# Kernel optimization log

Hardware: AMD Instinct MI355X
Metric: run time of the kernel (lower is better)

The kernel has to match this reference:

```python
import math
import jax, jax.numpy as jnp
import numpy as np

B, C, T, N, H = 4, 512, 2048, 4096, 4


def setup_inputs() -> dict:
    key = jax.random.key(0)
    ks = jax.random.split(key, 6)
    w = lambda k, shape: jax.random.normal(k, shape, dtype=jnp.float32) * 0.02
    return {
        "hidden_states": jax.random.normal(ks[0], (B, C, T), dtype=jnp.float32),
        "codebook_hidden_states": jax.random.normal(ks[1], (N, C), dtype=jnp.float32),
        # Linear weights stored as (in, out) so application is x @ W + b
        "Wq": w(ks[2], (C, C)), "bq": jnp.zeros((C,), jnp.float32),
        "Wk": w(ks[3], (C, C)), "bk": jnp.zeros((C,), jnp.float32),
        "Wv": w(ks[4], (C, C)), "bv": jnp.zeros((C,), jnp.float32),
        "Wp": w(ks[5], (C, H)), "bp": jnp.zeros((H,), jnp.float32),
    }


def reference(hidden_states, codebook_hidden_states, Wq, bq, Wk, bk, Wv, bv, Wp, bp):
    b, c, t = hidden_states.shape
    n = codebook_hidden_states.shape[0]
    h = bp.shape[0]
    d = c // h
    hs = hidden_states.transpose(0, 2, 1)                               # [B,T,C]
    q = (hs @ Wq + bq).reshape(b, t, h, d).transpose(0, 2, 1, 3)        # [B,H,T,d]
    k = (codebook_hidden_states @ Wk + bk).reshape(n, h, d).transpose(1, 0, 2)  # [H,N,d]
    v = codebook_hidden_states @ Wv + bv                                # [N,C]
    cg = hs @ Wp + bp                                                   # [B,T,H] head-pool gates
    scale = 1.0 / math.sqrt(d)
    logits_h = jnp.einsum('bhtd,hnd->bhnt', q, k) * scale               # [B,H,N,T]
    logits = jnp.einsum('bth,bhnt->bnt', cg, logits_h) / math.sqrt(h)   # [B,N,T]
    soft = jax.nn.softmax(logits, axis=1)                               # over codebook axis N
    idx = jnp.argmax(soft, axis=1)                                      # [B,T]
    hard = jax.nn.one_hot(idx, n, dtype=logits.dtype).transpose(0, 2, 1)  # [B,N,T]
    # straight-through: value == hard, gradient flows through soft
    one_hot = soft + jax.lax.stop_gradient(hard - soft)
    z_q = jnp.einsum('bnt,nd->bdt', one_hot, v)                         # [B,C,T]
    return logits, idx[:, None, :], z_q
```

## Files before the change

### kernel.cpp

```cpp
#include <hip/hip_runtime.h>
#include <hip/hip_bf16.h>
#include <cstddef>
#include <cstdint>

#define BB 4
#define CC 512
#define TT 2048
#define NN 4096
#define HH 4

constexpr float KFAC       = 0.04419417382415922f;
constexpr float INV_S18    = 1.0f / 262144.0f;
constexpr float INV_SCALE2 = 1.0f / (512.0f * 512.0f);

typedef _Float16 f16x8 __attribute__((ext_vector_type(8)));
typedef _Float16 f16x4 __attribute__((ext_vector_type(4)));
typedef float    f32x4 __attribute__((ext_vector_type(4)));

__device__ __forceinline__ void gld16(const void* g, void* s) {
    __builtin_amdgcn_global_load_lds(
        (const __attribute__((address_space(1))) void*)g,
        (__attribute__((address_space(3))) void*)s, 16, 0, 0);
}

struct HL { _Float16 h, l; };
__device__ __forceinline__ HL split512(float x) {
    float v = x * 512.0f;
    _Float16 h = (_Float16)v;
    return { h, (_Float16)(v - (float)h) };
}

__global__ __launch_bounds__(256) void k_split(
    const float* __restrict__ src, _Float16* __restrict__ hi, _Float16* __restrict__ lo, int n4)
{
    int q = blockIdx.x * 256 + threadIdx.x;
    if (q >= n4) return;
    float4 v = *(const float4*)(src + (size_t)q * 4);
    f16x4 H, L;
    HL a = split512(v.x); H[0] = a.h; L[0] = a.l;
    HL b = split512(v.y); H[1] = b.h; L[1] = b.l;
    HL c = split512(v.z); H[2] = c.h; L[2] = c.l;
    HL d = split512(v.w); H[3] = d.h; L[3] = d.l;
    *(f16x4*)(hi + (size_t)q * 4) = H;
    *(f16x4*)(lo + (size_t)q * 4) = L;
}

__device__ __forceinline__ void tsplit_body(
    const float* __restrict__ src, _Float16* __restrict__ hi, _Float16* __restrict__ lo,
    int S, int R, int r0, int s0)
{
    __shared__ float ls[64][65];
    const int tid = threadIdx.x;
    #pragma unroll
    for (int i = 0; i < 4; ++i) {
        int q = tid + i * 256;
        int row = q >> 4, c4 = (q & 15) * 4;
        float4 v = *(const float4*)(src + (size_t)(r0 + row) * S + s0 + c4);
        ls[row][c4] = v.x; ls[row][c4 + 1] = v.y;
        ls[row][c4 + 2] = v.z; ls[row][c4 + 3] = v.w;
    }
    __syncthreads();
    #pragma unroll
    for (int i = 0; i < 2; ++i) {
        int q = tid + i * 256;
        int orow = q >> 3, seg = (q & 7) * 8;
        f16x8 H, L;
        #pragma unroll
        for (int j = 0; j < 8; ++j) {
            HL s = split512(ls[seg + j][orow]);
            H[j] = s.h; L[j] = s.l;
        }
        size_t off = (size_t)(s0 + orow) * R + r0 + seg;
        *(f16x8*)(hi + off) = H;
        *(f16x8*)(lo + off) = L;
    }
}

__global__ __launch_bounds__(256) void k_tsplit(
    const float* __restrict__ src, _Float16* __restrict__ hi, _Float16* __restrict__ lo,
    long sbatch, long dbatch, int S, int R)
{
    src += (size_t)blockIdx.z * sbatch;
    hi  += (size_t)blockIdx.z * dbatch;
    lo  += (size_t)blockIdx.z * dbatch;
    tsplit_body(src, hi, lo, S, R, blockIdx.y * 64, blockIdx.x * 64);
}

__global__ __launch_bounds__(256) void k_tsplit_w(
    const float* __restrict__ w0, const float* __restrict__ w1, const float* __restrict__ w2,
    _Float16* __restrict__ h0, _Float16* __restrict__ h1, _Float16* __restrict__ h2,
    _Float16* __restrict__ l0, _Float16* __restrict__ l1, _Float16* __restrict__ l2)
{
    const int z = blockIdx.z;
    const float* src = z == 0 ? w0 : z == 1 ? w1 : w2;
    _Float16* hi = z == 0 ? h0 : z == 1 ? h1 : h2;
    _Float16* lo = z == 0 ? l0 : z == 1 ? l1 : l2;
    tsplit_body(src, hi, lo, CC, CC, blockIdx.y * 64, blockIdx.x * 64);
}

#define MFMA_TILE_DECLS                                                       \
    __shared__ __align__(16) _Float16 Ah[128][32];                            \
    __shared__ __align__(16) _Float16 Al[128][32];                            \
    __shared__ __align__(16) _Float16 Bh[128][32];                            \
    __shared__ __align__(16) _Float16 Bl[128][32];                            \
    const int tid  = threadIdx.x;                                             \
    const int w    = tid >> 6;                                                \
    const int l    = tid & 63;                                                \
    const int quad = l >> 4;                                                  \
    const int l15  = l & 15;                                                  \
    const int wm   = (w >> 1) * 64;                                           \
    const int wn   = (w & 1) * 64;                                            \
    const int rA   = l >> 2;                                                  \
    const int cA   = (l & 3) * 8;                                             \
    f32x4 acc[4][4];                                                          \
    _Pragma("unroll") for (int i = 0; i < 4; ++i)                             \
        _Pragma("unroll") for (int j = 0; j < 4; ++j)                         \
            acc[i][j] = (f32x4){0.f, 0.f, 0.f, 0.f};

#define MFMA_TILE_STAGE(pAh, pAl, pBh, pBl, k0, srcStride)                    \
    gld16(pAh + k0,                    &Ah[w * 32][0]);                       \
    gld16(pAh + k0 + 16 * (srcStride), &Ah[w * 32 + 16][0]);                  \
    gld16(pAl + k0,                    &Al[w * 32][0]);                       \
    gld16(pAl + k0 + 16 * (srcStride), &Al[w * 32 + 16][0]);                  \
    gld16(pBh + k0,                    &Bh[w * 32][0]);                       \
    gld16(pBh + k0 + 16 * (srcStride), &Bh[w * 32 + 16][0]);                  \
    gld16(pBl + k0,                    &Bl[w * 32][0]);                       \
    gld16(pBl + k0 + 16 * (srcStride), &Bl[w * 32 + 16][0]);

#define MFMA_TILE_COMPUTE                                                     \
    {                                                                         \
        f16x8 fah[4], fal[4], fbh[4], fbl[4];                                 \
        _Pragma("unroll") for (int i = 0; i < 4; ++i) {                       \
            fah[i] = *(const f16x8*)&Ah[wm + i * 16 + l15][quad * 8];         \
            fal[i] = *(const f16x8*)&Al[wm + i * 16 + l15][quad * 8];         \
            fbh[i] = *(const f16x8*)&Bh[wn + i * 16 + l15][quad * 8];         \
            fbl[i] = *(const f16x8*)&Bl[wn + i * 16 + l15][quad * 8];         \
        }                                                                     \
        _Pragma("unroll") for (int i = 0; i < 4; ++i)                         \
            _Pragma("unroll") for (int j = 0; j < 4; ++j) {                   \
                acc[i][j] = __builtin_amdgcn_mfma_f32_16x16x32_f16(fah[i], fbh[j], acc[i][j], 0, 0, 0); \
                acc[i][j] = __builtin_amdgcn_mfma_f32_16x16x32_f16(fah[i], fbl[j], acc[i][j], 0, 0, 0); \
                acc[i][j] = __builtin_amdgcn_mfma_f32_16x16x32_f16(fal[i], fbh[j], acc[i][j], 0, 0, 0); \
            }                                                                 \
    }

__global__ __launch_bounds__(256, 2) void k_proj_all(
    const _Float16* __restrict__ hsTh, const _Float16* __restrict__ hsTl,
    const _Float16* __restrict__ cbhi, const _Float16* __restrict__ cblo,
    const _Float16* __restrict__ wqTh, const _Float16* __restrict__ wqTl,
    const _Float16* __restrict__ wkTh, const _Float16* __restrict__ wkTl,
    const _Float16* __restrict__ wvTh, const _Float16* __restrict__ wvTl,
    const float* __restrict__ bq, const float* __restrict__ bk, const float* __restrict__ bv,
    const float* __restrict__ Wp, const float* __restrict__ bp,
    _Float16* __restrict__ qhi, _Float16* __restrict__ qlo,
    _Float16* __restrict__ khi, _Float16* __restrict__ klo, float* __restrict__ vproj)
{
    const int z    = blockIdx.z;
    const int y    = blockIdx.y;
    const int c0   = blockIdx.x * 128;
    const int path = z == 0 ? 0 : (y < 32 ? 1 : 2);
    const int m0   = (z == 0 ? y : (y & 31)) * 128;
    const int hblk = c0 >> 7;

    const _Float16* srcAh = z == 0 ? hsTh : cbhi;
    const _Float16* srcAl = z == 0 ? hsTl : cblo;
    const _Float16* bTh   = path == 0 ? wqTh : path == 1 ? wkTh : wvTh;
    const _Float16* bTl   = path == 0 ? wqTl : path == 1 ? wkTl : wvTl;
    const float*    bias  = path == 0 ? bq   : path == 1 ? bk   : bv;

    MFMA_TILE_DECLS
    __shared__ float wp_sh[32];
    __shared__ float gate_sh[128];
    float gate = 0.f;

    const _Float16* pAh = srcAh + (size_t)(m0 + w * 32 + rA) * CC + cA;
    const _Float16* pAl = srcAl + (size_t)(m0 + w * 32 + rA) * CC + cA;
    const _Float16* pBh = bTh   + (size_t)(c0 + w * 32 + rA) * CC + cA;
    const _Float16* pBl = bTl   + (size_t)(c0 + w * 32 + rA) * CC + cA;

    for (int k0 = 0; k0 < CC; k0 += 32) {
        MFMA_TILE_STAGE(pAh, pAl, pBh, pBl, k0, CC)
        if (path == 0 && tid < 32) wp_sh[tid] = Wp[(size_t)(k0 + tid) * HH + hblk];
        __syncthreads();
        MFMA_TILE_COMPUTE
        if (path == 0 && tid < 128) {
            #pragma unroll
            for (int s = 0; s < 4; ++s) {
                f16x8 hv = *(const f16x8*)&Ah[tid][s * 8];
                f16x8 lv = *(const f16x8*)&Al[tid][s * 8];
                #pragma unroll
                for (int jj = 0; jj < 8; ++jj)
                    gate = fmaf((float)hv[jj] + (float)lv[jj], wp_sh[s * 8 + jj], gate);
            }
        }
        __syncthreads();
    }

    if (path == 0) {
        if (tid < 128)
            gate_sh[tid] = (gate * (1.0f / 512.0f) + bp[hblk]) * KFAC;
        __syncthreads();
        #pragma unroll
        for (int i = 0; i < 4; ++i)
            #pragma unroll
            for (int j = 0; j < 4; ++j) {
                int col = c0 + wn + j * 16 + l15;
                float bi = bias[col];
                #pragma unroll
                for (int r = 0; r < 4; ++r) {
                    int rloc = wm + i * 16 + quad * 4 + r;
                    float v = fmaf(acc[i][j][r], INV_S18, bi) * gate_sh[rloc];
                    HL s = split512(v);
                    qhi[(size_t)(m0 + rloc) * CC + col] = s.h;
                    qlo[(size_t)(m0 + rloc) * CC + col] = s.l;
                }
            }
    } else if (path == 1) {
        #pragma unroll
        for (int i = 0; i < 4; ++i)
            #pragma unroll
            for (int j = 0; j < 4; ++j) {
                int col = c0 + wn + j * 16 + l15;
                float bi = bias[col];
                #pragma unroll
                for (int r = 0; r < 4; ++r) {
                    int row = m0 + wm + i * 16 + quad * 4 + r;
                    float v = fmaf(acc[i][j][r], INV_S18, bi);
                    HL s = split512(v);
                    khi[(size_t)row * CC + col] = s.h;
                    klo[(size_t)row * CC + col] = s.l;
                }
            }
    } else {
        #pragma unroll
        for (int i = 0; i < 4; ++i)
            #pragma unroll
            for (int j = 0; j < 4; ++j) {
                int col = c0 + wn + j * 16 + l15;
                float bi = bias[col];
                #pragma unroll
                for (int r = 0; r < 4; ++r) {
                    int row = m0 + wm + i * 16 + quad * 4 + r;
                    vproj[(size_t)row * CC + col] = fmaf(acc[i][j][r], INV_S18, bi);
                }
            }
    }
}

__global__ __launch_bounds__(256, 2) void k_logits_mfma(
    const _Float16* __restrict__ khi, const _Float16* __restrict__ klo,
    const _Float16* __restrict__ qhi, const _Float16* __restrict__ qlo,
    float* __restrict__ logits,
    float* __restrict__ pval,
    int*   __restrict__ pidx)
{
    const int b  = blockIdx.z;
    const int t0 = blockIdx.x * 128;
    const int n0 = blockIdx.y * 128;

    MFMA_TILE_DECLS
    __shared__ float rval[128];
    __shared__ int   ridx[128];

    const _Float16* pAh = khi + (size_t)(n0 + w * 32 + rA) * CC + cA;
    const _Float16* pAl = klo + (size_t)(n0 + w * 32 + rA) * CC + cA;
    const _Float16* pBh = qhi + ((size_t)b * TT + t0 + w * 32 + rA) * CC + cA;
    const _Float16* pBl = qlo + ((size_t)b * TT + t0 + w * 32 + rA) * CC + cA;

    for (int k0 = 0; k0 < CC; k0 += 32) {
        MFMA_TILE_STAGE(pAh, pAl, pBh, pBl, k0, CC)
        __syncthreads();
        MFMA_TILE_COMPUTE
        __syncthreads();
    }

    float bvj[4]; int bnj[4];
    #pragma unroll
    for (int j = 0; j < 4; ++j) {
        int col = t0 + wn + j * 16 + l15;
        float bv = -3.0e38f; int bn = 0;
        #pragma unroll
        for (int i = 0; i < 4; ++i) {
            #pragma unroll
            for (int r = 0; r < 4; ++r) {
                int row = n0 + wm + i * 16 + quad * 4 + r;
                float v = acc[i][j][r] * INV_SCALE2;
                logits[((size_t)b * NN + row) * TT + col] = v;
                if (v > bv) { bv = v; bn = row; }
            }
        }
        #pragma unroll
        for (int m = 16; m <= 32; m <<= 1) {
            float ov = __shfl_xor(bv, m, 64);
            int   on = __shfl_xor(bn, m, 64);
            if (ov > bv || (ov == bv && on < bn)) { bv = ov; bn = on; }
        }
        bvj[j] = bv; bnj[j] = bn;
    }
    if (w >= 2 && l < 16) {
        #pragma unroll
        for (int j = 0; j < 4; ++j) {
            rval[wn + j * 16 + l] = bvj[j];
            ridx[wn + j * 16 + l] = bnj[j];
        }
    }
    __syncthreads();
    if (w < 2 && l < 16) {
        #pragma unroll
        for (int j = 0; j < 4; ++j) {
            int cl = wn + j * 16 + l;
            float bv = bvj[j]; int bn = bnj[j];
            float ov = rval[cl];
            if (ov > bv) { bv = ov; bn = ridx[cl]; }
            size_t o = ((size_t)b * 32 + (n0 >> 7)) * TT + t0 + cl;
            pval[o] = bv;
            pidx[o] = bn;
        }
    }
}

__global__ __launch_bounds__(256) void k_finalize(
    const float* __restrict__ pval,
    const int*   __restrict__ pidx,
    const float* __restrict__ vproj,
    float* __restrict__ idx_out,
    float* __restrict__ zq)
{
    const int b  = blockIdx.y;
    const int t0 = blockIdx.x * 32;
    const int tid = threadIdx.x;

    __shared__ int sfin[32];
    if (tid < 32) {
        const int t = t0 + tid;
        float bv = -3.0e38f; int bn = 0;
        #pragma unroll
        for (int k = 0; k < 32; ++k) {
            size_t o = ((size_t)b * 32 + k) * TT + t;
            float v = pval[o];
            if (v > bv) { bv = v; bn = pidx[o]; }
        }
        idx_out[(size_t)b * TT + t] = (float)bn;
        sfin[tid] = bn;
    }
    __syncthreads();
    for (int pos = tid; pos < 32 * CC; pos += 256) {
        int c = pos >> 5, tl = pos & 31;
        zq[((size_t)b * CC + c) * TT + t0 + tl] = vproj[(size_t)sfin[tl] * CC + c];
    }
}

extern "C" void kernel_launch(void* const* d_in, const int* in_sizes, int n_in,
                              void* d_out, int out_size, void* d_ws, size_t ws_size,
                              hipStream_t stream)
{
    (void)in_sizes; (void)n_in; (void)out_size; (void)ws_size;
    const float* hs = (const float*)d_in[0];
    const float* cb = (const float*)d_in[1];
    const float* Wq = (const float*)d_in[2];
    const float* bq = (const float*)d_in[3];
    const float* Wk = (const float*)d_in[4];
    const float* bk = (const float*)d_in[5];
    const float* Wv = (const float*)d_in[6];
    const float* bv = (const float*)d_in[7];
    const float* Wp = (const float*)d_in[8];
    const float* bp = (const float*)d_in[9];

    char* ws = (char*)d_ws;
    const size_t MB = 1024 * 1024;
    _Float16* hsTh = (_Float16*)(ws);
    _Float16* hsTl = (_Float16*)(ws + 8  * MB);
    _Float16* qhi  = (_Float16*)(ws + 16 * MB);
    _Float16* qlo  = (_Float16*)(ws + 24 * MB);
    _Float16* cbhi = (_Float16*)(ws + 32 * MB);
    _Float16* cblo = (_Float16*)(ws + 36 * MB);
    _Float16* khi  = (_Float16*)(ws + 40 * MB);
    _Float16* klo  = (_Float16*)(ws + 44 * MB);
    float*    vproj= (float*)   (ws + 48 * MB);
    _Float16* wqTh = (_Float16*)(ws + 56 * MB);
    _Float16* wqTl = (_Float16*)(ws + 56 * MB + 524288);
    _Float16* wkTh = (_Float16*)(ws + 57 * MB);
    _Float16* wkTl = (_Float16*)(ws + 57 * MB + 524288);
    _Float16* wvTh = (_Float16*)(ws + 58 * MB);
    _Float16* wvTl = (_Float16*)(ws + 58 * MB + 524288);
    float* pval = (float*)(ws + 32 * MB);
    int*   pidx = (int*)  (ws + 33 * MB);

    float* logits = (float*)d_out;
    float* idxf   = logits + (size_t)BB * NN * TT;
    float* zq     = idxf + (size_t)BB * TT;

    k_split<<<dim3((NN * CC / 4 + 255) / 256), 256, 0, stream>>>(
        cb, cbhi, cblo, NN * CC / 4);
    k_tsplit<<<dim3(TT / 64, CC / 64, BB), 256, 0, stream>>>(
        hs, hsTh, hsTl, (long)CC * TT, (long)TT * CC, TT, CC);
    k_tsplit_w<<<dim3(CC / 64, CC / 64, 3), 256, 0, stream>>>(
        Wq, Wk, Wv, wqTh, wkTh, wvTh, wqTl, wkTl, wvTl);

    k_proj_all<<<dim3(CC / 128, 64, 2), 256, 0, stream>>>(
        hsTh, hsTl, cbhi, cblo,
        wqTh, wqTl, wkTh, wkTl, wvTh, wvTl,
        bq, bk, bv, Wp, bp,
        qhi, qlo, khi, klo, vproj);

    k_logits_mfma<<<dim3(TT / 128, NN / 128, BB), 256, 0, stream>>>(
        khi, klo, qhi, qlo, logits, pval, pidx);

    k_finalize<<<dim3(TT / 32, BB), 256, 0, stream>>>(
        pval, pidx, vproj, idxf, zq);
}
```

Baseline: 336.7 us.

## Rewrite logits GEMM as 256x256 tile, 8-wave ping-pong pipelined MFMA kernel

The logits GEMM moves from 128x128 tiles with 4 waves and synchronous staging to 256x256 tiles with 8 waves. It double-buffers LDS via global_load_lds, uses swizzled LDS offsets, interleaves the next tile's loads with MFMA sub-blocks under explicit barriers and s_setprio, and remaps blocks for locality. The split-fp16 hi/lo terms are now treated as extra K-tiles (24 K tiles total). The intent is to hide memory latency and raise MFMA utilisation and data reuse. The trade-off is 128 KB of LDS per block and high register pressure from 32 accumulators, which may limit occupancy.

```diff
diff --git a/kernel.cpp b/kernel.cpp
--- a/kernel.cpp
+++ b/kernel.cpp
@@ -247,48 +247,145 @@
     }
 }
 
-__global__ __launch_bounds__(256, 2) void k_logits_mfma(
+#define BAR   __builtin_amdgcn_s_barrier()
+#define LGKM0 { asm volatile("s_waitcnt lgkmcnt(0)" ::: "memory"); __builtin_amdgcn_sched_barrier(0); }
+#define PRIO1 __builtin_amdgcn_s_setprio(1)
+#define PRIO0 __builtin_amdgcn_s_setprio(0)
+
+#define STAGE_A(D, KT) {                                                      \
+    int sg_ = (KT) >> 3; int kof_ = ((KT) & 7) * 64;                          \
+    const _Float16* ab_ = (sg_ == 1 ? klo : khi) + arow0 + kof_;              \
+    gld16(ab_ + soff0,         &smem[(D) * 32768 + (w * 2 + 0) * 512]);       \
+    gld16(ab_ + soff1,         &smem[(D) * 32768 + (w * 2 + 1) * 512]);       \
+    gld16(ab_ + 65536 + soff0, &smem[(D) * 32768 + 8192 + (w * 2 + 0) * 512]);\
+    gld16(ab_ + 65536 + soff1, &smem[(D) * 32768 + 8192 + (w * 2 + 1) * 512]);\
+}
+#define STAGE_B(D, KT) {                                                      \
+    int sg_ = (KT) >> 3; int kof_ = ((KT) & 7) * 64;                          \
+    const _Float16* bb_ = (sg_ == 2 ? qlo : qhi) + brow0 + kof_;              \
+    gld16(bb_ + soff0,         &smem[(D) * 32768 + 16384 + (w * 2 + 0) * 512]);\
+    gld16(bb_ + soff1,         &smem[(D) * 32768 + 16384 + (w * 2 + 1) * 512]);\
+    gld16(bb_ + 65536 + soff0, &smem[(D) * 32768 + 24576 + (w * 2 + 0) * 512]);\
+    gld16(bb_ + 65536 + soff1, &smem[(D) * 32768 + 24576 + (w * 2 + 1) * 512]);\
+}
+#define RD_A(D, HF) {                                                         \
+    _Pragma("unroll") for (int ii = 0; ii < 4; ++ii)                          \
+      _Pragma("unroll") for (int kk = 0; kk < 2; ++kk)                        \
+        ah[ii][kk] = *(const f16x8*)&smem[(D) * 32768 + ha * 8192 +           \
+                         ((HF) * 4 + ii) * 1024 + kk * 32 + rdoffh];          \
+}
+#define RD_B(D, HF) {                                                         \
+    _Pragma("unroll") for (int jj = 0; jj < 2; ++jj)                          \
+      _Pragma("unroll") for (int kk = 0; kk < 2; ++kk)                        \
+        bf[(HF) * 2 + jj][kk] = *(const f16x8*)&smem[(D) * 32768 + 16384 +    \
+            hb * 8192 + wb64f + ((HF) * 2 + jj) * 1024 + kk * 32 + rdoffh];   \
+}
+#define MM(AH, BH) {                                                          \
+    _Pragma("unroll") for (int kk = 0; kk < 2; ++kk)                          \
+      _Pragma("unroll") for (int ii = 0; ii < 4; ++ii)                        \
+        _Pragma("unroll") for (int jj = 0; jj < 2; ++jj)                      \
+          acc[(AH) * 4 + ii][(BH) * 2 + jj] =                                 \
+            __builtin_amdgcn_mfma_f32_16x16x32_f16(ah[ii][kk],                \
+                bf[(BH) * 2 + jj][kk], acc[(AH) * 4 + ii][(BH) * 2 + jj], 0, 0, 0); \
+}
+#define KTILE(D, KTN, DOSTAGE) {                                              \
+    if (DOSTAGE) STAGE_A(1 - (D), KTN);                                       \
+    RD_A(D, 0); RD_B(D, 0);                                                   \
+    BAR; LGKM0; PRIO1; MM(0, 0); PRIO0; BAR;                                  \
+    if (DOSTAGE) STAGE_B(1 - (D), KTN);                                       \
+    RD_B(D, 1);                                                               \
+    BAR; LGKM0; PRIO1; MM(0, 1); PRIO0; BAR;                                  \
+    RD_A(D, 1);                                                               \
+    BAR; LGKM0; PRIO1; MM(1, 1); PRIO0; BAR;                                  \
+    PRIO1; MM(1, 0); PRIO0;                                                   \
+    if (DOSTAGE) { asm volatile("s_waitcnt vmcnt(0)" ::: "memory"); }         \
+    BAR;                                                                      \
+}
+
+__global__ __launch_bounds__(512, 2) void k_logits_8p(
     const _Float16* __restrict__ khi, const _Float16* __restrict__ klo,
     const _Float16* __restrict__ qhi, const _Float16* __restrict__ qlo,
     float* __restrict__ logits,
     float* __restrict__ pval,
     int*   __restrict__ pidx)
 {
-    const int b  = blockIdx.z;
-    const int t0 = blockIdx.x * 128;
-    const int n0 = blockIdx.y * 128;
-
-    MFMA_TILE_DECLS
-    __shared__ float rval[128];
-    __shared__ int   ridx[128];
-
-    const _Float16* pAh = khi + (size_t)(n0 + w * 32 + rA) * CC + cA;
-    const _Float16* pAl = klo + (size_t)(n0 + w * 32 + rA) * CC + cA;
-    const _Float16* pBh = qhi + ((size_t)b * TT + t0 + w * 32 + rA) * CC + cA;
-    const _Float16* pBl = qlo + ((size_t)b * TT + t0 + w * 32 + rA) * CC + cA;
-
-    for (int k0 = 0; k0 < CC; k0 += 32) {
-        MFMA_TILE_STAGE(pAh, pAl, pBh, pBl, k0, CC)
-        __syncthreads();
-        MFMA_TILE_COMPUTE
-        __syncthreads();
-    }
-
+    __shared__ __align__(16) _Float16 smem[65536];
+
+    const int f  = blockIdx.x + 8 * (blockIdx.y + 16 * blockIdx.z);
+    const int fs = (f & 7) * 64 + (f >> 3);
+    const int t0 = (fs & 7) * 256;
+    const int by = (fs >> 3) & 15;
+    const int b  = fs >> 7;
+    const int n0 = by * 256;
+
+    const int tid  = threadIdx.x;
+    const int w    = tid >> 6;
+    const int l    = tid & 63;
+    const int quad = l >> 4;
+    const int l15  = l & 15;
+    const int wm   = (w >> 2) * 128;
+    const int ha   = w >> 2;
+    const int wn   = (w & 3) * 64;
+    const int hb   = (w & 3) >> 1;
+    const int wb64f = (w & 1) * 4096;
+
+    const size_t arow0 = (size_t)n0 * CC;
+    const size_t brow0 = ((size_t)b * TT + t0) * CC;
+
+    size_t soff0, soff1;
+    {
+        int p0 = (w * 2 + 0) * 64 + l;
+        int s0 = p0 ^ (((p0 >> 5) & 1) << 1);
+        soff0 = (size_t)(s0 >> 3) * CC + (size_t)(s0 & 7) * 8;
+        int p1 = (w * 2 + 1) * 64 + l;
+        int s1 = p1 ^ (((p1 >> 5) & 1) << 1);
+        soff1 = (size_t)(s1 >> 3) * CC + (size_t)(s1 & 7) * 8;
+    }
+    const int rdoffh = (l15 * 64 + quad * 8) ^ ((((l15 >> 2) & 1)) << 4);
+
+    f32x4 acc[8][4];
+    #pragma unroll
+    for (int i = 0; i < 8; ++i)
+        #pragma unroll
+        for (int j = 0; j < 4; ++j)
+            acc[i][j] = (f32x4){0.f, 0.f, 0.f, 0.f};
+    f16x8 ah[4][2];
+    f16x8 bf[4][2];
+
+    STAGE_A(0, 0); STAGE_B(0, 0);
+    asm volatile("s_waitcnt vmcnt(0)" ::: "memory");
+    BAR;
+
+    for (int kt2 = 0; kt2 < 12; ++kt2) {
+        const int kt = kt2 * 2;
+        KTILE(0, kt + 1, 1);
+        KTILE(1, kt + 2, kt2 < 11);
+    }
+
+    {
+        const size_t lb = ((size_t)b * NN + n0 + wm) * TT + t0 + wn;
+        #pragma unroll
+        for (int i = 0; i < 8; ++i)
+            #pragma unroll
+            for (int r = 0; r < 4; ++r) {
+                const size_t rowoff = lb + (size_t)(i * 16 + quad * 4 + r) * TT;
+                #pragma unroll
+                for (int j = 0; j < 4; ++j)
+                    logits[rowoff + j * 16 + l15] = acc[i][j][r] * INV_SCALE2;
+            }
+    }
     float bvj[4]; int bnj[4];
     #pragma unroll
     for (int j = 0; j < 4; ++j) {
-        int col = t0 + wn + j * 16 + l15;
         float bv = -3.0e38f; int bn = 0;
         #pragma unroll
-        for (int i = 0; i < 4; ++i) {
+        for (int i = 0; i < 8; ++i)
             #pragma unroll
             for (int r = 0; r < 4; ++r) {
+                float v = acc[i][j][r] * INV_SCALE2;
                 int row = n0 + wm + i * 16 + quad * 4 + r;
-                float v = acc[i][j][r] * INV_SCALE2;
-                logits[((size_t)b * NN + row) * TT + col] = v;
                 if (v > bv) { bv = v; bn = row; }
             }
-        }
         #pragma unroll
         for (int m = 16; m <= 32; m <<= 1) {
             float ov = __shfl_xor(bv, m, 64);
@@ -297,22 +394,25 @@
         }
         bvj[j] = bv; bnj[j] = bn;
     }
-    if (w >= 2 && l < 16) {
+    float* rv = (float*)smem;
+    int*   ri = (int*)(smem + 1024);
+    __syncthreads();
+    if (w >= 4 && l < 16) {
         #pragma unroll
         for (int j = 0; j < 4; ++j) {
-            rval[wn + j * 16 + l] = bvj[j];
-            ridx[wn + j * 16 + l] = bnj[j];
+            rv[wn + j * 16 + l] = bvj[j];
+            ri[wn + j * 16 + l] = bnj[j];
         }
     }
     __syncthreads();
-    if (w < 2 && l < 16) {
+    if (w < 4 && l < 16) {
         #pragma unroll
         for (int j = 0; j < 4; ++j) {
             int cl = wn + j * 16 + l;
             float bv = bvj[j]; int bn = bnj[j];
-            float ov = rval[cl];
-            if (ov > bv) { bv = ov; bn = ridx[cl]; }
-            size_t o = ((size_t)b * 32 + (n0 >> 7)) * TT + t0 + cl;
+            float ov = rv[cl];
+            if (ov > bv) { bv = ov; bn = ri[cl]; }
+            size_t o = ((size_t)b * 16 + by) * TT + t0 + cl;
             pval[o] = bv;
             pidx[o] = bn;
         }
@@ -335,8 +435,8 @@
         const int t = t0 + tid;
         float bv = -3.0e38f; int bn = 0;
         #pragma unroll
-        for (int k = 0; k < 32; ++k) {
-            size_t o = ((size_t)b * 32 + k) * TT + t;
+        for (int k = 0; k < 16; ++k) {
+            size_t o = ((size_t)b * 16 + k) * TT + t;
             float v = pval[o];
             if (v > bv) { bv = v; bn = pidx[o]; }
         }
@@ -403,7 +503,7 @@
         bq, bk, bv, Wp, bp,
         qhi, qlo, khi, klo, vproj);
 
-    k_logits_mfma<<<dim3(TT / 128, NN / 128, BB), 256, 0, stream>>>(
+    k_logits_8p<<<dim3(TT / 256, NN / 256, BB), 512, 0, stream>>>(
         khi, klo, qhi, qlo, logits, pval, pidx);
 
     k_finalize<<<dim3(TT / 32, BB), 256, 0, stream>>>(
```

Result: no change. 331.5 us (-1.5%).
